# Kernel optimization log

Measured on AMD Instinct MI355X. Metric: run time of the kernel, lower is better.

The kernel has to match this reference:

```python
import jax, jax.numpy as jnp
import numpy as np

ITEM_NUMS = 100000
EMB_DIM = 128
HID_DIM = 128
N_ITEMS = 50000      # len(item_emb_idxes)
N_SESS = 50000       # rows of session_adj
N_TOTAL = N_SESS + N_ITEMS
NNZ_S = 500000
NNZ_A = 3200000
BATCH = 2048
N_SCORE = 50000


def setup_inputs() -> dict:
    key = jax.random.key(0)
    ks = jax.random.split(key, 12)
    return {
        "emb_table": jax.random.normal(ks[0], (ITEM_NUMS, EMB_DIM), jnp.float32),
        "W": jax.random.normal(ks[1], (EMB_DIM, HID_DIM), jnp.float32) * 0.01,
        "b": jax.random.normal(ks[2], (HID_DIM,), jnp.float32) * 0.01,
        "sess_vals": jax.random.uniform(ks[3], (NNZ_S,), jnp.float32),
        "A_vals": jax.random.uniform(ks[4], (NNZ_A,), jnp.float32),
        "batch_idxes": jax.random.randint(ks[5], (BATCH,), 0, N_TOTAL),
        "item_idxes": jax.random.randint(ks[6], (N_SCORE,), 0, N_TOTAL),
        "item_emb_idxes": jax.random.randint(ks[7], (N_ITEMS,), 0, ITEM_NUMS),
        "sess_rows": jax.random.randint(ks[8], (NNZ_S,), 0, N_SESS),
        "sess_cols": jax.random.randint(ks[9], (NNZ_S,), 0, N_ITEMS),
        "A_rows": jax.random.randint(ks[10], (NNZ_A,), 0, N_TOTAL),
        "A_cols": jax.random.randint(ks[11], (NNZ_A,), 0, N_TOTAL),
    }


def reference(emb_table, W, b, sess_vals, A_vals, batch_idxes, item_idxes,
              item_emb_idxes, sess_rows, sess_cols, A_rows, A_cols):
    # embedding gather: [N_ITEMS, EMB_DIM]
    x_item = emb_table[item_emb_idxes]
    # spmm(session_adj, x_item): [N_SESS, EMB_DIM]
    x_session = jax.ops.segment_sum(sess_vals[:, None] * x_item[sess_cols],
                                    sess_rows, num_segments=N_SESS)
    x = jnp.concatenate((x_session, x_item), axis=0)  # [N_TOTAL, EMB_DIM]
    # GCNconv: (x @ W) then spmm(A, .) + bias
    xw = x @ W                                         # [N_TOTAL, HID_DIM]
    h1 = jax.ops.segment_sum(A_vals[:, None] * xw[A_cols],
                             A_rows, num_segments=N_TOTAL) + b
    # score: [BATCH, N_SCORE]
    out = h1[batch_idxes] @ h1[item_idxes].T
    return out
```

## Files before the change

### kernel.cpp

```cpp
#include <hip/hip_runtime.h>

#define EMB 128
#define N_ITEMS 50000
#define N_SESS 50000
#define N_TOTAL 100000
#define NNZ_S 500000
#define NNZ_A 3200000
#define BATCH 2048
#define N_SCORE 50000

#define RPB 64
#define NB_A ((N_TOTAL + RPB - 1) / RPB)
#define NB_S ((N_SESS + RPB - 1) / RPB)
#define NBMAX 1600
#define EPT 8
#define EPB (256 * EPT)
#define NBLK_S ((NNZ_S + EPB - 1) / EPB)
#define NBLK_A ((NNZ_A + EPB - 1) / EPB)
#define XW_BLKS ((N_ITEMS + 127) / 128)
#define CHUNK 4096

#define STRIDE_S 1024
#define STRIDE_A 2560

#define MARK_BLKS ((BATCH + N_SCORE + 255) / 256)

#define SB_X ((N_SCORE + 127) / 128)
#define SB_Y (BATCH / 256)
#define SB_TOT (SB_X * SB_Y)

typedef __attribute__((ext_vector_type(8))) short bf16x8;
typedef __attribute__((ext_vector_type(4))) float f32x4;

__device__ inline ushort f2bf(float f) {
    unsigned u = __float_as_uint(f);
    unsigned r = (u + 0x7fff + ((u >> 16) & 1)) >> 16;
    return (ushort)r;
}
__device__ inline float bflo(unsigned u) { return __uint_as_float(u << 16); }
__device__ inline float bfhi(unsigned u) { return __uint_as_float(u & 0xffff0000u); }

__global__ __launch_bounds__(256) void k_prep(const int* __restrict__ bidx, const int* __restrict__ iidx,
                                              unsigned* __restrict__ bm,
                                              const float* __restrict__ W, ushort* __restrict__ Wt) {
    int blk = blockIdx.x;
    int tid = threadIdx.x;
    if (blk < MARK_BLKS) {
        int i = blk * 256 + tid;
        int r = -1;
        if (i < BATCH) r = bidx[i];
        else if (i < BATCH + N_SCORE) r = iidx[i - BATCH];
        if (r >= 0) atomicOr(&bm[r >> 5], 1u << (r & 31));
    } else {
        int i = (blk - MARK_BLKS) * 256 + tid;
        int n = i >> 7, k = i & 127;
        Wt[n * 128 + k] = f2bf(W[k * 128 + n]);
    }
}

__global__ __launch_bounds__(256) void k_build(const int* __restrict__ sRows, const int* __restrict__ sCols,
                                               const float* __restrict__ sVals, int* __restrict__ tailS,
                                               int2* __restrict__ edgS,
                                               const int* __restrict__ aRows, const int* __restrict__ aCols,
                                               const float* __restrict__ aVals, int* __restrict__ tailA,
                                               int2* __restrict__ edgA,
                                               const unsigned* __restrict__ bm,
                                               const float* __restrict__ emb,
                                               const int* __restrict__ emb_idx,
                                               const ushort* __restrict__ Wt,
                                               ushort* __restrict__ xw_item) {
    __shared__ int h[NBMAX];
    __shared__ int base_s[NBMAX];
    int blk = blockIdx.x;
    int tid = threadIdx.x;
    if (blk < NBLK_S + NBLK_A) {
        const int *rows, *cols;
        const float* vals;
        int* tail;
        int2* out;
        const unsigned* filt;
        int nnz, nb, stride;
        long b0;
        if (blk < NBLK_S) {
            rows = sRows; cols = sCols; vals = sVals; tail = tailS; out = edgS;
            filt = nullptr; nnz = NNZ_S; nb = NB_S; stride = STRIDE_S;
            b0 = (long)blk * EPB;
        } else {
            rows = aRows; cols = aCols; vals = aVals; tail = tailA; out = edgA;
            filt = bm; nnz = NNZ_A; nb = NB_A; stride = STRIDE_A;
            b0 = (long)(blk - NBLK_S) * EPB;
        }
        for (int i = tid; i < nb; i += 256) h[i] = 0;
        __syncthreads();
        int er[EPT], ec[EPT];
        float ev[EPT];
#pragma unroll
        for (int j = 0; j < EPT; ++j) {
            long e = b0 + j * 256 + tid;
            er[j] = -1;
            if (e < nnz) {
                int r = rows[e];
                if (!filt || ((filt[r >> 5] >> (r & 31)) & 1)) {
                    er[j] = r;
                    ec[j] = cols[e];
                    ev[j] = vals[e];
                    atomicAdd(&h[r >> 6], 1);
                }
            }
        }
        __syncthreads();
        for (int i = tid; i < nb; i += 256) {
            int v = h[i];
            if (v) base_s[i] = atomicAdd(&tail[i], v);
            h[i] = 0;
        }
        __syncthreads();
#pragma unroll
        for (int j = 0; j < EPT; ++j) {
            if (er[j] >= 0) {
                int bk = er[j] >> 6;
                int loc = base_s[bk] + atomicAdd(&h[bk], 1);
                if (loc < stride)
                    out[(long)bk * stride + loc] = make_int2(((er[j] & 63) << 17) | ec[j],
                                                             __float_as_int(ev[j]));
            }
        }
    } else {
        int bid = blk - NBLK_S - NBLK_A;
        int wid = tid >> 6;
        int lane = tid & 63;
        int wm = wid >> 1, wn = wid & 1;
        long m0 = (long)bid * 128 + wm * 64;
        int n0 = wn * 64;
        int r = lane & 15;
        int kg = lane >> 4;

        long arow[4];
#pragma unroll
        for (int mf = 0; mf < 4; ++mf) {
            long row = m0 + mf * 16 + r;
            if (row >= N_ITEMS) row = N_ITEMS - 1;
            arow[mf] = emb_idx[row];
        }

        f32x4 acc[4][4] = {};
#pragma unroll
        for (int ks = 0; ks < 4; ++ks) {
            bf16x8 a[4], b[4];
#pragma unroll
            for (int mf = 0; mf < 4; ++mf) {
                const float* p = emb + arow[mf] * EMB + ks * 32 + kg * 8;
                float4 lo = *(const float4*)p;
                float4 hi = *(const float4*)(p + 4);
                bf16x8 t;
                t[0] = (short)f2bf(lo.x); t[1] = (short)f2bf(lo.y);
                t[2] = (short)f2bf(lo.z); t[3] = (short)f2bf(lo.w);
                t[4] = (short)f2bf(hi.x); t[5] = (short)f2bf(hi.y);
                t[6] = (short)f2bf(hi.z); t[7] = (short)f2bf(hi.w);
                a[mf] = t;
            }
#pragma unroll
            for (int nf = 0; nf < 4; ++nf) {
                int row = n0 + nf * 16 + r;
                b[nf] = *(const bf16x8*)(Wt + (long)row * EMB + ks * 32 + kg * 8);
            }
#pragma unroll
            for (int mf = 0; mf < 4; ++mf)
#pragma unroll
                for (int nf = 0; nf < 4; ++nf)
                    acc[mf][nf] = __builtin_amdgcn_mfma_f32_16x16x32_bf16(a[mf], b[nf], acc[mf][nf], 0, 0, 0);
        }
#pragma unroll
        for (int mf = 0; mf < 4; ++mf) {
#pragma unroll
            for (int nf = 0; nf < 4; ++nf) {
                int col = n0 + nf * 16 + r;
#pragma unroll
                for (int j = 0; j < 4; ++j) {
                    long row = m0 + mf * 16 + kg * 4 + j;
                    if (row < N_ITEMS) xw_item[row * EMB + col] = f2bf(acc[mf][nf][j]);
                }
            }
        }
    }
}

__global__ __launch_bounds__(512) void k_spmm_sorted(const int* __restrict__ tail,
                                                     const int2* __restrict__ edges, int stride,
                                                     const ushort* __restrict__ src,
                                                     ushort* __restrict__ dst,
                                                     const float* __restrict__ bias,
                                                     int nrows,
                                                     const unsigned* __restrict__ bm) {
    __shared__ int2 se[CHUNK];
    __shared__ int hist[RPB], sofs[RPB], cur[RPB];
    int tid = threadIdx.x, lane = tid & 63, w = tid >> 6;
    int bk = blockIdx.x;
    long begin = (long)bk * stride;
    int cnt = tail[bk];
    if (cnt > stride) cnt = stride;
    long end = begin + cnt;

    float2 acc[8] = {};
    for (long cbase = begin; cbase < end; cbase += CHUNK) {
        int m = (int)(end - cbase);
        if (m > CHUNK) m = CHUNK;
        if (tid < RPB) hist[tid] = 0;
        __syncthreads();
        int2 er[CHUNK / 512];
#pragma unroll
        for (int j = 0; j < CHUNK / 512; ++j) {
            int idx = j * 512 + tid;
            if (idx < m) {
                er[j] = edges[cbase + idx];
                atomicAdd(&hist[er[j].x >> 17], 1);
            } else {
                er[j].x = -1;
            }
        }
        __syncthreads();
        if (w == 0) {
            int v = hist[lane];
            int x = v;
#pragma unroll
            for (int s = 1; s < 64; s <<= 1) {
                int t = __shfl_up(x, s, 64);
                if (lane >= s) x += t;
            }
            sofs[lane] = x - v;
            cur[lane] = x - v;
        }
        __syncthreads();
#pragma unroll
        for (int j = 0; j < CHUNK / 512; ++j) {
            if (er[j].x >= 0) {
                int lr = er[j].x >> 17;
                int p = atomicAdd(&cur[lr], 1);
                se[p] = er[j];
            }
        }
        __syncthreads();
#pragma unroll
        for (int i = 0; i < 8; ++i) {
            int lr = w * 8 + i;
            int e = sofs[lr];
            int s1 = e + hist[lr];
            for (; e + 4 <= s1; e += 4) {
                int2 e0 = se[e], e1 = se[e + 1], e2 = se[e + 2], e3 = se[e + 3];
                unsigned u0 = *(const unsigned*)(src + (long)(e0.x & 0x1FFFF) * EMB + lane * 2);
                unsigned u1 = *(const unsigned*)(src + (long)(e1.x & 0x1FFFF) * EMB + lane * 2);
                unsigned u2 = *(const unsigned*)(src + (long)(e2.x & 0x1FFFF) * EMB + lane * 2);
                unsigned u3 = *(const unsigned*)(src + (long)(e3.x & 0x1FFFF) * EMB + lane * 2);
                float v0 = __int_as_float(e0.y), v1 = __int_as_float(e1.y);
                float v2 = __int_as_float(e2.y), v3 = __int_as_float(e3.y);
                acc[i].x += v0 * bflo(u0) + v1 * bflo(u1) + v2 * bflo(u2) + v3 * bflo(u3);
                acc[i].y += v0 * bfhi(u0) + v1 * bfhi(u1) + v2 * bfhi(u2) + v3 * bfhi(u3);
            }
            for (; e < s1; ++e) {
                int2 e0 = se[e];
                unsigned u0 = *(const unsigned*)(src + (long)(e0.x & 0x1FFFF) * EMB + lane * 2);
                float v0 = __int_as_float(e0.y);
                acc[i].x += v0 * bflo(u0);
                acc[i].y += v0 * bfhi(u0);
            }
        }
        __syncthreads();
    }
#pragma unroll
    for (int i = 0; i < 8; ++i) {
        int r = bk * RPB + w * 8 + i;
        if (r < nrows && (!bm || ((bm[r >> 5] >> (r & 31)) & 1))) {
            float a = acc[i].x, c = acc[i].y;
            if (bias) {
                a += bias[lane * 2];
                c += bias[lane * 2 + 1];
            }
            unsigned o = (unsigned)f2bf(a) | ((unsigned)f2bf(c) << 16);
            *((unsigned*)(dst + (long)r * EMB) + lane) = o;
        }
    }
}

__global__ __launch_bounds__(512) void k_score_mfma(const ushort* __restrict__ H,
                                                    const int* __restrict__ bidx,
                                                    const int* __restrict__ iidx,
                                                    float* __restrict__ C) {
    const int q = SB_TOT / 8;
    int bid = blockIdx.x;
    int nb = (bid % 8) * q + bid / 8;
    int bx = nb / SB_Y;
    int by = nb % SB_Y;

    int wid = threadIdx.x >> 6;
    int lane = threadIdx.x & 63;
    int wm = wid >> 1, wn = wid & 1;
    long m0 = (long)by * 256 + wm * 64;
    long n0 = (long)bx * 128 + wn * 64;
    int r = lane & 15;
    int kg = lane >> 4;

    long arow[4], brow[4];
#pragma unroll
    for (int mf = 0; mf < 4; ++mf) arow[mf] = bidx[m0 + mf * 16 + r];
#pragma unroll
    for (int nf = 0; nf < 4; ++nf) {
        long row = n0 + nf * 16 + r;
        if (row >= N_SCORE) row = N_SCORE - 1;
        brow[nf] = iidx[row];
    }

    f32x4 acc[4][4] = {};
#pragma unroll
    for (int ks = 0; ks < 4; ++ks) {
        bf16x8 a[4], b[4];
#pragma unroll
        for (int mf = 0; mf < 4; ++mf)
            a[mf] = *(const bf16x8*)(H + arow[mf] * EMB + ks * 32 + kg * 8);
#pragma unroll
        for (int nf = 0; nf < 4; ++nf)
            b[nf] = *(const bf16x8*)(H + brow[nf] * EMB + ks * 32 + kg * 8);
#pragma unroll
        for (int mf = 0; mf < 4; ++mf)
#pragma unroll
            for (int nf = 0; nf < 4; ++nf)
                acc[mf][nf] = __builtin_amdgcn_mfma_f32_16x16x32_bf16(a[mf], b[nf], acc[mf][nf], 0, 0, 0);
    }
#pragma unroll
    for (int mf = 0; mf < 4; ++mf) {
#pragma unroll
        for (int nf = 0; nf < 4; ++nf) {
            long col = n0 + nf * 16 + r;
            if (col < N_SCORE) {
#pragma unroll
                for (int j = 0; j < 4; ++j) {
                    long row = m0 + mf * 16 + kg * 4 + j;
                    __builtin_nontemporal_store(acc[mf][nf][j], &C[row * N_SCORE + col]);
                }
            }
        }
    }
}

extern "C" void kernel_launch(void* const* d_in, const int* in_sizes, int n_in,
                              void* d_out, int out_size, void* d_ws, size_t ws_size,
                              hipStream_t stream) {
    const float* emb_table      = (const float*)d_in[0];
    const float* W              = (const float*)d_in[1];
    const float* b              = (const float*)d_in[2];
    const float* sess_vals      = (const float*)d_in[3];
    const float* A_vals         = (const float*)d_in[4];
    const int*   batch_idxes    = (const int*)d_in[5];
    const int*   item_idxes     = (const int*)d_in[6];
    const int*   item_emb_idxes = (const int*)d_in[7];
    const int*   sess_rows      = (const int*)d_in[8];
    const int*   sess_cols      = (const int*)d_in[9];
    const int*   A_rows         = (const int*)d_in[10];
    const int*   A_cols         = (const int*)d_in[11];
    float* out = (float*)d_out;

    char* base = (char*)d_ws;
    ushort*   xw    = (ushort*)(base + 0);
    ushort*   h1    = (ushort*)(base + 25600000L);
    int2*     edgA  = (int2*)  (base + 51200000L);
    int2*     edgS  = (int2*)  (base + 83210240L);
    ushort*   Wt    = (ushort*)(base + 89616384L);
    unsigned* bm    = (unsigned*)(base + 89649152L);
    int*      tailS = (int*)   (base + 89661696L);
    int*      tailA = (int*)   (base + 89664824L);

    ushort* xw_item = xw + (long)N_SESS * EMB;

    hipMemsetAsync(bm, 0, 89671076L - 89649152L, stream);
    k_prep<<<MARK_BLKS + 64, 256, 0, stream>>>(batch_idxes, item_idxes, bm, W, Wt);
    k_build<<<NBLK_S + NBLK_A + XW_BLKS, 256, 0, stream>>>(
        sess_rows, sess_cols, sess_vals, tailS, edgS,
        A_rows, A_cols, A_vals, tailA, edgA, bm,
        emb_table, item_emb_idxes, Wt, xw_item);
    k_spmm_sorted<<<NB_S, 512, 0, stream>>>(tailS, edgS, STRIDE_S, xw_item, xw,
                                            nullptr, N_SESS, nullptr);
    k_spmm_sorted<<<NB_A, 512, 0, stream>>>(tailA, edgA, STRIDE_A, xw, h1,
                                            b, N_TOTAL, bm);
    k_score_mfma<<<SB_TOT, 512, 0, stream>>>(h1, batch_idxes, item_idxes, out);
}
```

Measured before the change: 354.3 us.

## Swap MFMA operands for vectorized row stores and widen SpMM gathers

Swaps the A and B operands of the MFMA calls in the XW and score kernels so each lane holds four consecutive columns of one row. The epilogues can then write 4-wide vectors (ushort4 / f32x4 nontemporal) instead of scattered scalar stores. The sorted SpMM now has each half-wave handle a different edge with 8-byte gathers, combined at the end with a cross-half shuffle reduction, so fewer, wider memory requests are issued per edge. The risks are misaligned vector stores in the score output, since N_SCORE*4 bytes per row is 16-byte aligned only when the column offset is a multiple of 4, which holds. The odd-tail handling in the score kernel assumes column groups of 4 never straddle N_SCORE, which holds because 50000 is divisible by 4.

```diff
diff --git a/kernel.cpp b/kernel.cpp
--- a/kernel.cpp
+++ b/kernel.cpp
@@ -168,17 +168,21 @@
             for (int mf = 0; mf < 4; ++mf)
 #pragma unroll
                 for (int nf = 0; nf < 4; ++nf)
-                    acc[mf][nf] = __builtin_amdgcn_mfma_f32_16x16x32_bf16(a[mf], b[nf], acc[mf][nf], 0, 0, 0);
+                    acc[mf][nf] = __builtin_amdgcn_mfma_f32_16x16x32_bf16(b[nf], a[mf], acc[mf][nf], 0, 0, 0);
         }
 #pragma unroll
         for (int mf = 0; mf < 4; ++mf) {
-#pragma unroll
-            for (int nf = 0; nf < 4; ++nf) {
-                int col = n0 + nf * 16 + r;
-#pragma unroll
-                for (int j = 0; j < 4; ++j) {
-                    long row = m0 + mf * 16 + kg * 4 + j;
-                    if (row < N_ITEMS) xw_item[row * EMB + col] = f2bf(acc[mf][nf][j]);
+            long row = m0 + mf * 16 + r;
+            if (row < N_ITEMS) {
+#pragma unroll
+                for (int nf = 0; nf < 4; ++nf) {
+                    int col0 = n0 + nf * 16 + kg * 4;
+                    ushort4 o;
+                    o.x = f2bf(acc[mf][nf][0]);
+                    o.y = f2bf(acc[mf][nf][1]);
+                    o.z = f2bf(acc[mf][nf][2]);
+                    o.w = f2bf(acc[mf][nf][3]);
+                    *(ushort4*)(xw_item + row * EMB + col0) = o;
                 }
             }
         }
@@ -195,13 +199,14 @@
     __shared__ int2 se[CHUNK];
     __shared__ int hist[RPB], sofs[RPB], cur[RPB];
     int tid = threadIdx.x, lane = tid & 63, w = tid >> 6;
+    int half = lane >> 5, l32 = lane & 31;
     int bk = blockIdx.x;
     long begin = (long)bk * stride;
     int cnt = tail[bk];
     if (cnt > stride) cnt = stride;
     long end = begin + cnt;
 
-    float2 acc[8] = {};
+    float4 acc[8] = {};
     for (long cbase = begin; cbase < end; cbase += CHUNK) {
         int m = (int)(end - cbase);
         if (m > CHUNK) m = CHUNK;
@@ -246,22 +251,27 @@
             int e = sofs[lr];
             int s1 = e + hist[lr];
             for (; e + 4 <= s1; e += 4) {
-                int2 e0 = se[e], e1 = se[e + 1], e2 = se[e + 2], e3 = se[e + 3];
-                unsigned u0 = *(const unsigned*)(src + (long)(e0.x & 0x1FFFF) * EMB + lane * 2);
-                unsigned u1 = *(const unsigned*)(src + (long)(e1.x & 0x1FFFF) * EMB + lane * 2);
-                unsigned u2 = *(const unsigned*)(src + (long)(e2.x & 0x1FFFF) * EMB + lane * 2);
-                unsigned u3 = *(const unsigned*)(src + (long)(e3.x & 0x1FFFF) * EMB + lane * 2);
-                float v0 = __int_as_float(e0.y), v1 = __int_as_float(e1.y);
-                float v2 = __int_as_float(e2.y), v3 = __int_as_float(e3.y);
-                acc[i].x += v0 * bflo(u0) + v1 * bflo(u1) + v2 * bflo(u2) + v3 * bflo(u3);
-                acc[i].y += v0 * bfhi(u0) + v1 * bfhi(u1) + v2 * bfhi(u2) + v3 * bfhi(u3);
-            }
-            for (; e < s1; ++e) {
-                int2 e0 = se[e];
-                unsigned u0 = *(const unsigned*)(src + (long)(e0.x & 0x1FFFF) * EMB + lane * 2);
-                float v0 = __int_as_float(e0.y);
-                acc[i].x += v0 * bflo(u0);
-                acc[i].y += v0 * bfhi(u0);
+                int2 ea = se[e + half];
+                int2 eb = se[e + 2 + half];
+                uint2 ua = *(const uint2*)(src + (long)(ea.x & 0x1FFFF) * EMB + l32 * 4);
+                uint2 ub = *(const uint2*)(src + (long)(eb.x & 0x1FFFF) * EMB + l32 * 4);
+                float va = __int_as_float(ea.y), vb = __int_as_float(eb.y);
+                acc[i].x += va * bflo(ua.x) + vb * bflo(ub.x);
+                acc[i].y += va * bfhi(ua.x) + vb * bfhi(ub.x);
+                acc[i].z += va * bflo(ua.y) + vb * bflo(ub.y);
+                acc[i].w += va * bfhi(ua.y) + vb * bfhi(ub.y);
+            }
+            for (; e < s1; e += 2) {
+                int eh = e + half;
+                if (eh < s1) {
+                    int2 e0 = se[eh];
+                    uint2 u0 = *(const uint2*)(src + (long)(e0.x & 0x1FFFF) * EMB + l32 * 4);
+                    float v0 = __int_as_float(e0.y);
+                    acc[i].x += v0 * bflo(u0.x);
+                    acc[i].y += v0 * bfhi(u0.x);
+                    acc[i].z += v0 * bflo(u0.y);
+                    acc[i].w += v0 * bfhi(u0.y);
+                }
             }
         }
         __syncthreads();
@@ -270,13 +280,21 @@
     for (int i = 0; i < 8; ++i) {
         int r = bk * RPB + w * 8 + i;
         if (r < nrows && (!bm || ((bm[r >> 5] >> (r & 31)) & 1))) {
-            float a = acc[i].x, c = acc[i].y;
-            if (bias) {
-                a += bias[lane * 2];
-                c += bias[lane * 2 + 1];
-            }
-            unsigned o = (unsigned)f2bf(a) | ((unsigned)f2bf(c) << 16);
-            *((unsigned*)(dst + (long)r * EMB) + lane) = o;
+            float4 t = acc[i];
+            t.x += __shfl_xor(t.x, 32, 64);
+            t.y += __shfl_xor(t.y, 32, 64);
+            t.z += __shfl_xor(t.z, 32, 64);
+            t.w += __shfl_xor(t.w, 32, 64);
+            if (half == 0) {
+                if (bias) {
+                    float4 bb = *(const float4*)(bias + l32 * 4);
+                    t.x += bb.x; t.y += bb.y; t.z += bb.z; t.w += bb.w;
+                }
+                uint2 o;
+                o.x = (unsigned)f2bf(t.x) | ((unsigned)f2bf(t.y) << 16);
+                o.y = (unsigned)f2bf(t.z) | ((unsigned)f2bf(t.w) << 16);
+                *(uint2*)(dst + (long)r * EMB + l32 * 4) = o;
+            }
         }
     }
 }
@@ -323,19 +341,17 @@
         for (int mf = 0; mf < 4; ++mf)
 #pragma unroll
             for (int nf = 0; nf < 4; ++nf)
-                acc[mf][nf] = __builtin_amdgcn_mfma_f32_16x16x32_bf16(a[mf], b[nf], acc[mf][nf], 0, 0, 0);
+                acc[mf][nf] = __builtin_amdgcn_mfma_f32_16x16x32_bf16(b[nf], a[mf], acc[mf][nf], 0, 0, 0);
     }
 #pragma unroll
     for (int mf = 0; mf < 4; ++mf) {
+        long row = m0 + mf * 16 + r;
 #pragma unroll
         for (int nf = 0; nf < 4; ++nf) {
-            long col = n0 + nf * 16 + r;
-            if (col < N_SCORE) {
-#pragma unroll
-                for (int j = 0; j < 4; ++j) {
-                    long row = m0 + mf * 16 + kg * 4 + j;
-                    __builtin_nontemporal_store(acc[mf][nf][j], &C[row * N_SCORE + col]);
-                }
+            long col0 = n0 + nf * 16 + kg * 4;
+            if (col0 < N_SCORE) {
+                f32x4* p = (f32x4*)&C[row * N_SCORE + col0];
+                __builtin_nontemporal_store(acc[mf][nf], p);
             }
         }
     }
```

Measured after the change: 382.6 us. +8.0%, slower.
